# Optimization experiments

Hardware: AMD Instinct MI355X
Metric: run time of the kernel (lower is better)

The kernel has to match this reference:

```python
import jax, jax.numpy as jnp
import numpy as np

POS_DIM = 3
LATENT = 128
HEADS = 4
HEAD_DIM = LATENT // HEADS
KERNEL_IN = 4 * POS_DIM - POS_DIM + 1  # q_pos,o_pos,rel,dist -> 10
N_Q = 1024
N_O = 2048
LN_EPS = 1e-5


def setup_inputs() -> dict:
    key = jax.random.key(0)
    ks = jax.random.split(key, 9)
    s = lambda fan_in: 1.0 / np.sqrt(fan_in)
    return {
        "h_obs": jax.random.normal(ks[0], (N_O, LATENT), dtype=jnp.float32),
        "pos_obs": jax.random.normal(ks[1], (N_O, POS_DIM), dtype=jnp.float32),
        "pos_query": jax.random.normal(ks[2], (N_Q, POS_DIM), dtype=jnp.float32),
        "obs_batch": jnp.zeros((N_O,), dtype=jnp.int32),
        "query_batch": jnp.zeros((N_Q,), dtype=jnp.int32),
        # kernel_mlp: Linear(10, 128) -> ReLU -> Linear(128, 4); stored as [in, out]
        "W1": jax.random.uniform(ks[3], (KERNEL_IN, LATENT), jnp.float32, -s(KERNEL_IN), s(KERNEL_IN)),
        "b1": jnp.zeros((LATENT,), jnp.float32),
        "W2": jax.random.uniform(ks[4], (LATENT, HEADS), jnp.float32, -s(LATENT), s(LATENT)),
        "b2": jnp.zeros((HEADS,), jnp.float32),
        "ln_gamma": jnp.ones((LATENT,), jnp.float32),
        "ln_beta": jnp.zeros((LATENT,), jnp.float32),
        "Wv": jax.random.uniform(ks[5], (LATENT, LATENT), jnp.float32, -s(LATENT), s(LATENT)),
        "bv": jnp.zeros((LATENT,), jnp.float32),
    }


def reference(h_obs, pos_obs, pos_query, obs_batch, query_batch,
              W1, b1, W2, b2, ln_gamma, ln_beta, Wv, bv):
    N_q, N_o = pos_query.shape[0], pos_obs.shape[0]
    # pairwise relative position encodings: [N_q, N_o, 10]
    rel = pos_query[:, None, :] - pos_obs[None, :, :]            # [N_q, N_o, P]
    dist = jnp.linalg.norm(rel, axis=-1, keepdims=True)          # [N_q, N_o, 1]
    pos_q_exp = jnp.broadcast_to(pos_query[:, None, :], rel.shape)
    pos_o_exp = jnp.broadcast_to(pos_obs[None, :, :], rel.shape)
    kernel_input = jnp.concatenate([pos_q_exp, pos_o_exp, rel, dist], axis=-1)
    # per-pair MLP score -> logits [N_q, N_o, H]
    hidden = jax.nn.relu(jnp.einsum('qok,kl->qol', kernel_input, W1) + b1)
    logits = jnp.einsum('qol,lh->qoh', hidden, W2) + b2
    # same-graph mask (softmax over N_o axis)
    batch_mask = query_batch[:, None] == obs_batch[None, :]      # [N_q, N_o]
    logits = jnp.where(batch_mask[:, :, None], logits, -jnp.inf)
    weights = jax.nn.softmax(logits, axis=1)                     # over N_o
    # value path: LayerNorm -> value_proj -> heads
    mu = jnp.mean(h_obs, axis=-1, keepdims=True)
    var = jnp.var(h_obs, axis=-1, keepdims=True)
    h_norm = (h_obs - mu) * jax.lax.rsqrt(var + LN_EPS) * ln_gamma + ln_beta
    v = (h_norm @ Wv + bv).reshape(N_o, HEADS, HEAD_DIM)         # [N_o, H, D]
    # weighted aggregation: [N_q, H, D] -> [N_q, latent]
    h_query = jnp.einsum('qoh,ohd->qhd', weights, v)
    return h_query.reshape(N_q, LATENT)
```

## Files before the change

### kernel.cpp

```cpp
#include <hip/hip_runtime.h>

#define NQ 1024
#define NO 2048
#define LAT 128
#define CHUNK 16
#define NCHUNK (NO / CHUNK)
#define LOG2E 1.4426950408889634f
#define NEG_BIG -3.0e38f
#define MASK_THRESH -1.0e37f
#define PART_STRIDE 136
#define SY_MAX 32

__global__ __launch_bounds__(256) void gano_value(
    const float* __restrict__ ln_g,
    const float* __restrict__ ln_b,
    const float* __restrict__ Wv,
    const float* __restrict__ bv,
    float* __restrict__ h)
{
    __shared__ float hn[LAT];
    __shared__ float red[8];
    __shared__ float part[LAT];
    const int t = threadIdx.x;
    const int o = blockIdx.x;
    const int d = t & 127;
    const int kh = t >> 7;

    const float x = h[(size_t)o*LAT + d];
    float s1 = x, s2 = x*x;
#pragma unroll
    for (int off = 32; off >= 1; off >>= 1) {
        s1 += __shfl_xor(s1, off);
        s2 += __shfl_xor(s2, off);
    }
    const int w = t >> 6;
    if ((t & 63) == 0) { red[w*2] = s1; red[w*2+1] = s2; }
    __syncthreads();
    const float S1 = red[0] + red[2];
    const float S2 = red[1] + red[3];
    const float mean = S1 * (1.0f/LAT);
    const float var  = S2 * (1.0f/LAT) - mean*mean;
    const float rstd = rsqrtf(var + 1e-5f);
    if (t < LAT)
        hn[d] = (x - mean) * rstd * ln_g[d] + ln_b[d];
    __syncthreads();

    float acc = kh ? 0.f : bv[d];
    const float* wp = Wv + (size_t)(kh*64)*LAT + d;
    const float* hp = hn + kh*64;
#pragma unroll 8
    for (int kk = 0; kk < 64; ++kk)
        acc = fmaf(hp[kk], wp[(size_t)kk*LAT], acc);
    if (kh) part[d] = acc;
    __syncthreads();
    if (!kh) h[(size_t)o*LAT + d] = acc + part[d];
}

__global__ __launch_bounds__(256) void gano_main(
    const float* __restrict__ v,
    const float* __restrict__ pos_obs,
    const float* __restrict__ pos_query,
    const int* __restrict__ obs_batch,
    const int* __restrict__ query_batch,
    const float* __restrict__ W1,
    const float* __restrict__ b1,
    const float* __restrict__ W2,
    const float* __restrict__ b2,
    float* __restrict__ ws,
    float* __restrict__ out,
    int SY)
{
    __shared__ __align__(16) float ld[CHUNK*LAT];
    __shared__ __align__(16) float lcq[16*LAT];
    __shared__ __align__(16) float lgt[16*4*CHUNK];
    __shared__ __align__(16) float w1d[3*LAT];
    __shared__ float lpos[CHUNK*3];
    __shared__ int   lob[CHUNK];

    const int tid = threadIdx.x;
    const int i  = tid & 15;
    const int qi = tid >> 4;
    const int q  = blockIdx.x * 16 + qi;
    const int d0 = i * 8;
    const int hstar = i >> 2;

    for (int idx = tid; idx < 3*LAT; idx += 256) {
        const int a = idx >> 7, dd = idx & 127;
        w1d[idx] = W1[(3+a)*LAT + dd] - W1[(6+a)*LAT + dd];
    }
#pragma unroll
    for (int t2 = 0; t2 < 2; ++t2) {
        const int idx = tid + t2*256;
        const int row = idx >> 5;
        const int g   = idx & 31;
        const int dd  = g * 4;
        const int qq  = blockIdx.x * 16 + row;
        const float px = pos_query[qq*3+0];
        const float py = pos_query[qq*3+1];
        const float pz = pos_query[qq*3+2];
        float4 c = *(const float4*)(b1 + dd);
        const float4 wx0 = *(const float4*)(W1 + 0*LAT + dd);
        const float4 wx6 = *(const float4*)(W1 + 6*LAT + dd);
        const float4 wy0 = *(const float4*)(W1 + 1*LAT + dd);
        const float4 wy6 = *(const float4*)(W1 + 7*LAT + dd);
        const float4 wz0 = *(const float4*)(W1 + 2*LAT + dd);
        const float4 wz6 = *(const float4*)(W1 + 8*LAT + dd);
        c.x = fmaf(px, wx0.x+wx6.x, fmaf(py, wy0.x+wy6.x, fmaf(pz, wz0.x+wz6.x, c.x)));
        c.y = fmaf(px, wx0.y+wx6.y, fmaf(py, wy0.y+wy6.y, fmaf(pz, wz0.y+wz6.y, c.y)));
        c.z = fmaf(px, wx0.z+wx6.z, fmaf(py, wy0.z+wy6.z, fmaf(pz, wz0.z+wz6.z, c.z)));
        c.w = fmaf(px, wx0.w+wx6.w, fmaf(py, wy0.w+wy6.w, fmaf(pz, wz0.w+wz6.w, c.w)));
        *(float4*)(lcq + row*LAT + ((g + row) & 31) * 4) = c;
    }

    const int   qb  = query_batch[q];

    float4 accA = make_float4(0.f,0.f,0.f,0.f);
    float4 accB = make_float4(0.f,0.f,0.f,0.f);
    float m = NEG_BIG, lsum = 0.f;

    for (int cb = blockIdx.y; cb < NCHUNK; cb += SY) {
        const int o0 = cb * CHUNK;
        __syncthreads();

        for (int idx = tid; idx < CHUNK*(LAT/4); idx += 256) {
            const int oo = idx >> 5;
            const int g  = idx & 31;
            const int d4 = g * 4;
            const float* po = pos_obs + (size_t)(o0 + oo)*3;
            const float px = po[0], py = po[1], pz = po[2];
            const float4 wa = *(const float4*)(w1d + 0*LAT + d4);
            const float4 wb = *(const float4*)(w1d + 1*LAT + d4);
            const float4 wc = *(const float4*)(w1d + 2*LAT + d4);
            float4 r;
            r.x = fmaf(px, wa.x, fmaf(py, wb.x, pz*wc.x));
            r.y = fmaf(px, wa.y, fmaf(py, wb.y, pz*wc.y));
            r.z = fmaf(px, wa.z, fmaf(py, wb.z, pz*wc.z));
            r.w = fmaf(px, wa.w, fmaf(py, wb.w, pz*wc.w));
            *(float4*)(ld + oo*LAT + ((g + oo) & 31) * 4) = r;
        }
        for (int idx = tid; idx < CHUNK*3; idx += 256) lpos[idx] = pos_obs[o0*3 + idx];
        for (int idx = tid; idx < CHUNK;   idx += 256) lob[idx]  = obs_batch[o0 + idx];
        __syncthreads();

        {
            const int oc = i;
            const float dx = pos_query[q*3+0] - lpos[oc*3+0];
            const float dy = pos_query[q*3+1] - lpos[oc*3+1];
            const float dz = pos_query[q*3+2] - lpos[oc*3+2];
            const float dist = sqrtf(dx*dx + dy*dy + dz*dz);
            const int mb = (lob[oc] == qb);

            float lg0 = 0.f, lg1 = 0.f, lg2 = 0.f, lg3 = 0.f;
            const float* ldr = ld + oc*LAT;
            const float* lcr = lcq + qi*LAT;
#pragma unroll 4
            for (int j = 0; j < 32; ++j) {
                const float4 dd = *(const float4*)(ldr + ((j + oc) & 31) * 4);
                const float4 cc = *(const float4*)(lcr + ((j + qi) & 31) * 4);
                const float4 wd = *(const float4*)(W1 + 9*LAT + j*4);
                const float4 w2a = *(const float4*)(W2 + (j*4+0)*4);
                const float4 w2b = *(const float4*)(W2 + (j*4+1)*4);
                const float4 w2c = *(const float4*)(W2 + (j*4+2)*4);
                const float4 w2d = *(const float4*)(W2 + (j*4+3)*4);
                const float h0 = fmaxf(fmaf(wd.x, dist, cc.x + dd.x), 0.f);
                const float h1 = fmaxf(fmaf(wd.y, dist, cc.y + dd.y), 0.f);
                const float h2 = fmaxf(fmaf(wd.z, dist, cc.z + dd.z), 0.f);
                const float h3 = fmaxf(fmaf(wd.w, dist, cc.w + dd.w), 0.f);
                lg0 = fmaf(h0, w2a.x, lg0); lg1 = fmaf(h0, w2a.y, lg1);
                lg2 = fmaf(h0, w2a.z, lg2); lg3 = fmaf(h0, w2a.w, lg3);
                lg0 = fmaf(h1, w2b.x, lg0); lg1 = fmaf(h1, w2b.y, lg1);
                lg2 = fmaf(h1, w2b.z, lg2); lg3 = fmaf(h1, w2b.w, lg3);
                lg0 = fmaf(h2, w2c.x, lg0); lg1 = fmaf(h2, w2c.y, lg1);
                lg2 = fmaf(h2, w2c.z, lg2); lg3 = fmaf(h2, w2c.w, lg3);
                lg0 = fmaf(h3, w2d.x, lg0); lg1 = fmaf(h3, w2d.y, lg1);
                lg2 = fmaf(h3, w2d.z, lg2); lg3 = fmaf(h3, w2d.w, lg3);
            }
            const int ocr = (oc + 4*qi) & 15;
            float* lrow = lgt + (qi*4)*CHUNK + ocr;
            lrow[0*CHUNK] = mb ? fmaf(lg0, LOG2E, b2[0]*LOG2E) : NEG_BIG;
            lrow[1*CHUNK] = mb ? fmaf(lg1, LOG2E, b2[1]*LOG2E) : NEG_BIG;
            lrow[2*CHUNK] = mb ? fmaf(lg2, LOG2E, b2[2]*LOG2E) : NEG_BIG;
            lrow[3*CHUNK] = mb ? fmaf(lg3, LOG2E, b2[3]*LOG2E) : NEG_BIG;
        }
        __syncthreads();

        {
            const float* rowp = lgt + (qi*4 + hstar)*CHUNK;
            float lgv[16];
#pragma unroll
            for (int p = 0; p < 4; ++p) {
                const float4 t = *(const float4*)(rowp + ((p + qi) & 3) * 4);
                lgv[p*4+0] = t.x; lgv[p*4+1] = t.y;
                lgv[p*4+2] = t.z; lgv[p*4+3] = t.w;
            }
#pragma unroll 4
            for (int oc = 0; oc < CHUNK; ++oc) {
                const float lg = lgv[oc];
                const float mn    = fmaxf(m, lg);
                const float alpha = exp2f(m - mn);
                const float p     = (lg > MASK_THRESH) ? exp2f(lg - mn) : 0.f;
                lsum = fmaf(lsum, alpha, p);
                m = mn;
                const float* vp = v + (size_t)(o0 + oc)*LAT + d0;
                const float4 vA = *(const float4*)vp;
                const float4 vB = *(const float4*)(vp + 4);
                accA.x = fmaf(accA.x, alpha, p*vA.x);
                accA.y = fmaf(accA.y, alpha, p*vA.y);
                accA.z = fmaf(accA.z, alpha, p*vA.z);
                accA.w = fmaf(accA.w, alpha, p*vA.w);
                accB.x = fmaf(accB.x, alpha, p*vB.x);
                accB.y = fmaf(accB.y, alpha, p*vB.y);
                accB.z = fmaf(accB.z, alpha, p*vB.z);
                accB.w = fmaf(accB.w, alpha, p*vB.w);
            }
        }
    }

    if (SY == 1) {
        const float inv = 1.0f / lsum;
        float* op = out + (size_t)q*LAT + d0;
        float4 rA, rB;
        rA.x = accA.x*inv; rA.y = accA.y*inv; rA.z = accA.z*inv; rA.w = accA.w*inv;
        rB.x = accB.x*inv; rB.y = accB.y*inv; rB.z = accB.z*inv; rB.w = accB.w*inv;
        *(float4*)op       = rA;
        *(float4*)(op + 4) = rB;
    } else {
        float* pp = ws + ((size_t)blockIdx.y * NQ + q) * PART_STRIDE;
        if ((i & 3) == 0) {
            pp[hstar]     = m;
            pp[4 + hstar] = lsum;
        }
        *(float4*)(pp + 8 + d0)     = accA;
        *(float4*)(pp + 8 + d0 + 4) = accB;
    }
}

__global__ __launch_bounds__(128) void gano_combine(
    const float* __restrict__ ws, float* __restrict__ out, int SY)
{
    const int q = blockIdx.x;
    const int l = threadIdx.x;
    const int h = l >> 5;
    float M = NEG_BIG, Ls = 0.f, A = 0.f;
    for (int s = 0; s < SY; ++s) {
        const float* pp = ws + ((size_t)s * NQ + q) * PART_STRIDE;
        const float ms = pp[h];
        const float ls = pp[4 + h];
        const float as = pp[8 + l];
        const float Mn = fmaxf(M, ms);
        const float a0 = exp2f(M - Mn);
        const float a1 = exp2f(ms - Mn);
        Ls = Ls*a0 + ls*a1;
        A  = A *a0 + as*a1;
        M = Mn;
    }
    out[(size_t)q*LAT + l] = A / Ls;
}

extern "C" void kernel_launch(void* const* d_in, const int* in_sizes, int n_in,
                              void* d_out, int out_size, void* d_ws, size_t ws_size,
                              hipStream_t stream) {
    (void)in_sizes; (void)n_in; (void)out_size;
    float*       h_obs     = (float*)d_in[0];
    const float* pos_obs   = (const float*)d_in[1];
    const float* pos_query = (const float*)d_in[2];
    const int*   obs_batch = (const int*)d_in[3];
    const int*   query_batch = (const int*)d_in[4];
    const float* W1 = (const float*)d_in[5];
    const float* b1 = (const float*)d_in[6];
    const float* W2 = (const float*)d_in[7];
    const float* b2 = (const float*)d_in[8];
    const float* ln_g = (const float*)d_in[9];
    const float* ln_b = (const float*)d_in[10];
    const float* Wv = (const float*)d_in[11];
    const float* bv = (const float*)d_in[12];
    float* ws  = (float*)d_ws;
    float* out = (float*)d_out;

    int SY = 1;
    const size_t per = (size_t)NQ * PART_STRIDE * sizeof(float);
    if (ws && ws_size >= 2*per) {
        size_t s = ws_size / per;
        SY = (int)(s < SY_MAX ? s : SY_MAX);
    }

    gano_value<<<NO, 256, 0, stream>>>(ln_g, ln_b, Wv, bv, h_obs);
    gano_main<<<dim3(NQ/16, SY), 256, 0, stream>>>(h_obs, pos_obs, pos_query,
                                                   obs_batch, query_batch,
                                                   W1, b1, W2, b2, ws, out, SY);
    if (SY > 1)
        gano_combine<<<NQ, 128, 0, stream>>>(ws, out, SY);
}
```

Measured before the change: 189.6 us.

## Batch online-softmax updates in groups of four and pad LDS rows

```diff
diff --git a/kernel.cpp b/kernel.cpp
--- a/kernel.cpp
+++ b/kernel.cpp
@@ -5,6 +5,7 @@
 #define LAT 128
 #define CHUNK 16
 #define NCHUNK (NO / CHUNK)
+#define LDSTR 132
 #define LOG2E 1.4426950408889634f
 #define NEG_BIG -3.0e38f
 #define MASK_THRESH -1.0e37f
@@ -56,7 +57,7 @@
     if (!kh) h[(size_t)o*LAT + d] = acc + part[d];
 }
 
-__global__ __launch_bounds__(256) void gano_main(
+__global__ __launch_bounds__(256, 7) void gano_main(
     const float* __restrict__ v,
     const float* __restrict__ pos_obs,
     const float* __restrict__ pos_query,
@@ -70,10 +71,9 @@
     float* __restrict__ out,
     int SY)
 {
-    __shared__ __align__(16) float ld[CHUNK*LAT];
-    __shared__ __align__(16) float lcq[16*LAT];
+    __shared__ __align__(16) float ld[CHUNK*LDSTR];
+    __shared__ __align__(16) float lcq[16*LDSTR];
     __shared__ __align__(16) float lgt[16*4*CHUNK];
-    __shared__ __align__(16) float w1d[3*LAT];
     __shared__ float lpos[CHUNK*3];
     __shared__ int   lob[CHUNK];
 
@@ -84,35 +84,36 @@
     const int d0 = i * 8;
     const int hstar = i >> 2;
 
-    for (int idx = tid; idx < 3*LAT; idx += 256) {
-        const int a = idx >> 7, dd = idx & 127;
-        w1d[idx] = W1[(3+a)*LAT + dd] - W1[(6+a)*LAT + dd];
-    }
 #pragma unroll
     for (int t2 = 0; t2 < 2; ++t2) {
         const int idx = tid + t2*256;
         const int row = idx >> 5;
         const int g   = idx & 31;
-        const int dd  = g * 4;
+        const int dd4 = g * 4;
         const int qq  = blockIdx.x * 16 + row;
         const float px = pos_query[qq*3+0];
         const float py = pos_query[qq*3+1];
         const float pz = pos_query[qq*3+2];
-        float4 c = *(const float4*)(b1 + dd);
-        const float4 wx0 = *(const float4*)(W1 + 0*LAT + dd);
-        const float4 wx6 = *(const float4*)(W1 + 6*LAT + dd);
-        const float4 wy0 = *(const float4*)(W1 + 1*LAT + dd);
-        const float4 wy6 = *(const float4*)(W1 + 7*LAT + dd);
-        const float4 wz0 = *(const float4*)(W1 + 2*LAT + dd);
-        const float4 wz6 = *(const float4*)(W1 + 8*LAT + dd);
+        float4 c = *(const float4*)(b1 + dd4);
+        const float4 wx0 = *(const float4*)(W1 + 0*LAT + dd4);
+        const float4 wx6 = *(const float4*)(W1 + 6*LAT + dd4);
+        const float4 wy0 = *(const float4*)(W1 + 1*LAT + dd4);
+        const float4 wy6 = *(const float4*)(W1 + 7*LAT + dd4);
+        const float4 wz0 = *(const float4*)(W1 + 2*LAT + dd4);
+        const float4 wz6 = *(const float4*)(W1 + 8*LAT + dd4);
         c.x = fmaf(px, wx0.x+wx6.x, fmaf(py, wy0.x+wy6.x, fmaf(pz, wz0.x+wz6.x, c.x)));
         c.y = fmaf(px, wx0.y+wx6.y, fmaf(py, wy0.y+wy6.y, fmaf(pz, wz0.y+wz6.y, c.y)));
         c.z = fmaf(px, wx0.z+wx6.z, fmaf(py, wy0.z+wy6.z, fmaf(pz, wz0.z+wz6.z, c.z)));
         c.w = fmaf(px, wx0.w+wx6.w, fmaf(py, wy0.w+wy6.w, fmaf(pz, wz0.w+wz6.w, c.w)));
-        *(float4*)(lcq + row*LAT + ((g + row) & 31) * 4) = c;
-    }
-
+        *(float4*)(lcq + row*LDSTR + dd4) = c;
+    }
+
+    const float pqx = pos_query[q*3+0];
+    const float pqy = pos_query[q*3+1];
+    const float pqz = pos_query[q*3+2];
     const int   qb  = query_batch[q];
+    const float b2l0 = b2[0]*LOG2E, b2l1 = b2[1]*LOG2E;
+    const float b2l2 = b2[2]*LOG2E, b2l3 = b2[3]*LOG2E;
 
     float4 accA = make_float4(0.f,0.f,0.f,0.f);
     float4 accB = make_float4(0.f,0.f,0.f,0.f);
@@ -122,21 +123,26 @@
         const int o0 = cb * CHUNK;
         __syncthreads();
 
-        for (int idx = tid; idx < CHUNK*(LAT/4); idx += 256) {
+#pragma unroll
+        for (int t2 = 0; t2 < 2; ++t2) {
+            const int idx = tid + t2*256;
             const int oo = idx >> 5;
             const int g  = idx & 31;
             const int d4 = g * 4;
             const float* po = pos_obs + (size_t)(o0 + oo)*3;
             const float px = po[0], py = po[1], pz = po[2];
-            const float4 wa = *(const float4*)(w1d + 0*LAT + d4);
-            const float4 wb = *(const float4*)(w1d + 1*LAT + d4);
-            const float4 wc = *(const float4*)(w1d + 2*LAT + d4);
+            const float4 w3 = *(const float4*)(W1 + 3*LAT + d4);
+            const float4 w4 = *(const float4*)(W1 + 4*LAT + d4);
+            const float4 w5 = *(const float4*)(W1 + 5*LAT + d4);
+            const float4 w6 = *(const float4*)(W1 + 6*LAT + d4);
+            const float4 w7 = *(const float4*)(W1 + 7*LAT + d4);
+            const float4 w8 = *(const float4*)(W1 + 8*LAT + d4);
             float4 r;
-            r.x = fmaf(px, wa.x, fmaf(py, wb.x, pz*wc.x));
-            r.y = fmaf(px, wa.y, fmaf(py, wb.y, pz*wc.y));
-            r.z = fmaf(px, wa.z, fmaf(py, wb.z, pz*wc.z));
-            r.w = fmaf(px, wa.w, fmaf(py, wb.w, pz*wc.w));
-            *(float4*)(ld + oo*LAT + ((g + oo) & 31) * 4) = r;
+            r.x = fmaf(px, w3.x-w6.x, fmaf(py, w4.x-w7.x, pz*(w5.x-w8.x)));
+            r.y = fmaf(px, w3.y-w6.y, fmaf(py, w4.y-w7.y, pz*(w5.y-w8.y)));
+            r.z = fmaf(px, w3.z-w6.z, fmaf(py, w4.z-w7.z, pz*(w5.z-w8.z)));
+            r.w = fmaf(px, w3.w-w6.w, fmaf(py, w4.w-w7.w, pz*(w5.w-w8.w)));
+            *(float4*)(ld + oo*LDSTR + d4) = r;
         }
         for (int idx = tid; idx < CHUNK*3; idx += 256) lpos[idx] = pos_obs[o0*3 + idx];
         for (int idx = tid; idx < CHUNK;   idx += 256) lob[idx]  = obs_batch[o0 + idx];
@@ -144,19 +150,19 @@
 
         {
             const int oc = i;
-            const float dx = pos_query[q*3+0] - lpos[oc*3+0];
-            const float dy = pos_query[q*3+1] - lpos[oc*3+1];
-            const float dz = pos_query[q*3+2] - lpos[oc*3+2];
+            const float dx = pqx - lpos[oc*3+0];
+            const float dy = pqy - lpos[oc*3+1];
+            const float dz = pqz - lpos[oc*3+2];
             const float dist = sqrtf(dx*dx + dy*dy + dz*dz);
             const int mb = (lob[oc] == qb);
 
             float lg0 = 0.f, lg1 = 0.f, lg2 = 0.f, lg3 = 0.f;
-            const float* ldr = ld + oc*LAT;
-            const float* lcr = lcq + qi*LAT;
+            const float* ldr = ld + oc*LDSTR;
+            const float* lcr = lcq + qi*LDSTR;
 #pragma unroll 4
             for (int j = 0; j < 32; ++j) {
-                const float4 dd = *(const float4*)(ldr + ((j + oc) & 31) * 4);
-                const float4 cc = *(const float4*)(lcr + ((j + qi) & 31) * 4);
+                const float4 dd = *(const float4*)(ldr + j*4);
+                const float4 cc = *(const float4*)(lcr + j*4);
                 const float4 wd = *(const float4*)(W1 + 9*LAT + j*4);
                 const float4 w2a = *(const float4*)(W2 + (j*4+0)*4);
                 const float4 w2b = *(const float4*)(W2 + (j*4+1)*4);
@@ -177,10 +183,10 @@
             }
             const int ocr = (oc + 4*qi) & 15;
             float* lrow = lgt + (qi*4)*CHUNK + ocr;
-            lrow[0*CHUNK] = mb ? fmaf(lg0, LOG2E, b2[0]*LOG2E) : NEG_BIG;
-            lrow[1*CHUNK] = mb ? fmaf(lg1, LOG2E, b2[1]*LOG2E) : NEG_BIG;
-            lrow[2*CHUNK] = mb ? fmaf(lg2, LOG2E, b2[2]*LOG2E) : NEG_BIG;
-            lrow[3*CHUNK] = mb ? fmaf(lg3, LOG2E, b2[3]*LOG2E) : NEG_BIG;
+            lrow[0*CHUNK] = mb ? fmaf(lg0, LOG2E, b2l0) : NEG_BIG;
+            lrow[1*CHUNK] = mb ? fmaf(lg1, LOG2E, b2l1) : NEG_BIG;
+            lrow[2*CHUNK] = mb ? fmaf(lg2, LOG2E, b2l2) : NEG_BIG;
+            lrow[3*CHUNK] = mb ? fmaf(lg3, LOG2E, b2l3) : NEG_BIG;
         }
         __syncthreads();
 
@@ -193,25 +199,37 @@
                 lgv[p*4+0] = t.x; lgv[p*4+1] = t.y;
                 lgv[p*4+2] = t.z; lgv[p*4+3] = t.w;
             }
-#pragma unroll 4
-            for (int oc = 0; oc < CHUNK; ++oc) {
-                const float lg = lgv[oc];
-                const float mn    = fmaxf(m, lg);
+#pragma unroll
+            for (int og = 0; og < 4; ++og) {
+                const float l0 = lgv[og*4+0], l1 = lgv[og*4+1];
+                const float l2 = lgv[og*4+2], l3 = lgv[og*4+3];
+                const float mg = fmaxf(fmaxf(l0, l1), fmaxf(l2, l3));
+                const float mn = fmaxf(m, mg);
                 const float alpha = exp2f(m - mn);
-                const float p     = (lg > MASK_THRESH) ? exp2f(lg - mn) : 0.f;
-                lsum = fmaf(lsum, alpha, p);
+                const float p0 = (l0 > MASK_THRESH) ? exp2f(l0 - mn) : 0.f;
+                const float p1 = (l1 > MASK_THRESH) ? exp2f(l1 - mn) : 0.f;
+                const float p2 = (l2 > MASK_THRESH) ? exp2f(l2 - mn) : 0.f;
+                const float p3 = (l3 > MASK_THRESH) ? exp2f(l3 - mn) : 0.f;
+                lsum = fmaf(lsum, alpha, (p0 + p1) + (p2 + p3));
                 m = mn;
-                const float* vp = v + (size_t)(o0 + oc)*LAT + d0;
-                const float4 vA = *(const float4*)vp;
-                const float4 vB = *(const float4*)(vp + 4);
-                accA.x = fmaf(accA.x, alpha, p*vA.x);
-                accA.y = fmaf(accA.y, alpha, p*vA.y);
-                accA.z = fmaf(accA.z, alpha, p*vA.z);
-                accA.w = fmaf(accA.w, alpha, p*vA.w);
-                accB.x = fmaf(accB.x, alpha, p*vB.x);
-                accB.y = fmaf(accB.y, alpha, p*vB.y);
-                accB.z = fmaf(accB.z, alpha, p*vB.z);
-                accB.w = fmaf(accB.w, alpha, p*vB.w);
+
+                const float* vp = v + (size_t)(o0 + og*4)*LAT + d0;
+                const float4 v0A = *(const float4*)(vp + 0*LAT);
+                const float4 v0B = *(const float4*)(vp + 0*LAT + 4);
+                const float4 v1A = *(const float4*)(vp + 1*LAT);
+                const float4 v1B = *(const float4*)(vp + 1*LAT + 4);
+                const float4 v2A = *(const float4*)(vp + 2*LAT);
+                const float4 v2B = *(const float4*)(vp + 2*LAT + 4);
+                const float4 v3A = *(const float4*)(vp + 3*LAT);
+                const float4 v3B = *(const float4*)(vp + 3*LAT + 4);
+                accA.x = fmaf(accA.x, alpha, fmaf(p0, v0A.x, fmaf(p1, v1A.x, fmaf(p2, v2A.x, p3*v3A.x))));
+                accA.y = fmaf(accA.y, alpha, fmaf(p0, v0A.y, fmaf(p1, v1A.y, fmaf(p2, v2A.y, p3*v3A.y))));
+                accA.z = fmaf(accA.z, alpha, fmaf(p0, v0A.z, fmaf(p1, v1A.z, fmaf(p2, v2A.z, p3*v3A.z))));
+                accA.w = fmaf(accA.w, alpha, fmaf(p0, v0A.w, fmaf(p1, v1A.w, fmaf(p2, v2A.w, p3*v3A.w))));
+                accB.x = fmaf(accB.x, alpha, fmaf(p0, v0B.x, fmaf(p1, v1B.x, fmaf(p2, v2B.x, p3*v3B.x))));
+                accB.y = fmaf(accB.y, alpha, fmaf(p0, v0B.y, fmaf(p1, v1B.y, fmaf(p2, v2B.y, p3*v3B.y))));
+                accB.z = fmaf(accB.z, alpha, fmaf(p0, v0B.z, fmaf(p1, v1B.z, fmaf(p2, v2B.z, p3*v3B.z))));
+                accB.w = fmaf(accB.w, alpha, fmaf(p0, v0B.w, fmaf(p1, v1B.w, fmaf(p2, v2B.w, p3*v3B.w))));
             }
         }
     }
```

Result: slower. 650.0 us (+242.8%).
